# Kernel tuning notes

Measured on AMD Instinct MI355X. Metric: run time of the kernel, lower is better.

## Reference

```python
import jax, jax.numpy as jnp
import numpy as np
import math

N, IN_DIM, OUT_DIM = 4096, 1024, 1024
MASK = True


def setup_inputs() -> dict:
    key = jax.random.key(0)
    ks = jax.random.split(key, 6)
    s = 1.0 / math.sqrt(IN_DIM)
    return {
        "qx": jax.random.normal(ks[0], (N, IN_DIM), jnp.float32),
        "kx": jax.random.normal(ks[1], (N, IN_DIM), jnp.float32),
        "vx": jax.random.normal(ks[2], (N, IN_DIM), jnp.float32),
        # torch nn.Linear weight layout: [out_dim, in_dim], y = x @ W.T
        "Wq": jax.random.normal(ks[3], (OUT_DIM, IN_DIM), jnp.float32) * s,
        "Wk": jax.random.normal(ks[4], (OUT_DIM, IN_DIM), jnp.float32) * s,
        "Wv": jax.random.normal(ks[5], (OUT_DIM, IN_DIM), jnp.float32) * s,
    }


def reference(qx, kx, vx, Wq, Wk, Wv):
    q = qx @ Wq.T  # [n, d]
    k = kx @ Wk.T
    v = vx @ Wv.T
    scores = (q @ k.T) / jnp.float32(math.sqrt(OUT_DIM))  # [n, n]
    if MASK:
        n = qx.shape[0]
        col = jnp.arange(n)[None, :]
        row = jnp.arange(n)[:, None]
        # original: -10000 where j > i (strictly upper triangular)
        scores = scores + jnp.where(col > row, jnp.float32(-10000.0), jnp.float32(0.0))
    attn = jax.nn.softmax(scores, axis=1)
    return attn @ v
```

## Files before the change

### kernel.cpp

```cpp
#include <hip/hip_runtime.h>
#include <hip/hip_bf16.h>
#include <stdint.h>

#define NTOK 4096
#define DIM  1024

typedef unsigned short u16;
typedef __bf16 bf16x8 __attribute__((ext_vector_type(8)));
typedef float f32x4 __attribute__((ext_vector_type(4)));
typedef u16 u16x8 __attribute__((ext_vector_type(8)));

__device__ __forceinline__ u16 f2bf(float f) {
  union { float f; uint32_t u; } c; c.f = f;
  return (u16)((c.u + 0x7fffu + ((c.u >> 16) & 1u)) >> 16);
}
__device__ __forceinline__ float bf2f(u16 b) {
  union { uint32_t u; float f; } c; c.u = (uint32_t)b << 16;
  return c.f;
}

__device__ __forceinline__ float wave_max(float v) {
#pragma unroll
  for (int o = 32; o; o >>= 1) v = fmaxf(v, __shfl_xor(v, o, 64));
  return v;
}
__device__ __forceinline__ float wave_sum(float v) {
#pragma unroll
  for (int o = 32; o; o >>= 1) v += __shfl_xor(v, o, 64);
  return v;
}

__device__ __forceinline__ int xcd_swz(int orig, int nwg) {
  const int q = nwg >> 3, r = nwg & 7;
  const int x = orig & 7, i = orig >> 3;
  return (x < r ? x * (q + 1) : r * (q + 1) + (x - r) * q) + i;
}

__device__ __forceinline__ void gld16(const u16* g, u16* l) {
  __builtin_amdgcn_global_load_lds((const __attribute__((address_space(1))) void*)g,
                                   (__attribute__((address_space(3))) void*)l, 16, 0, 0);
}

template<int N> __device__ __forceinline__ void wait_vmcnt() {
  if constexpr (N == 0) asm volatile("s_waitcnt vmcnt(0)" ::: "memory");
  else if constexpr (N == 6) asm volatile("s_waitcnt vmcnt(6)" ::: "memory");
  else if constexpr (N == 8) asm volatile("s_waitcnt vmcnt(8)" ::: "memory");
}

__global__ __launch_bounds__(256) void cvt6(
    const float* __restrict__ qx, const float* __restrict__ kx, const float* __restrict__ vx,
    const float* __restrict__ Wq, const float* __restrict__ Wk, const float* __restrict__ Wv,
    u16* __restrict__ qxb, u16* __restrict__ kxb, u16* __restrict__ vxb,
    u16* __restrict__ Wqb, u16* __restrict__ Wkb, u16* __restrict__ Wvb)
{
  const int z = blockIdx.z;
  const int nelem = (z < 3) ? NTOK * DIM : DIM * DIM;
  const int i = (blockIdx.x * 256 + threadIdx.x) * 8;
  if (i >= nelem) return;
  const float* in = (z == 0) ? qx : (z == 1) ? kx : (z == 2) ? vx
                  : (z == 3) ? Wq : (z == 4) ? Wk : Wv;
  u16* out = (z == 0) ? qxb : (z == 1) ? kxb : (z == 2) ? vxb
           : (z == 3) ? Wqb : (z == 4) ? Wkb : Wvb;
  float4 a = *reinterpret_cast<const float4*>(in + i);
  float4 b = *reinterpret_cast<const float4*>(in + i + 4);
  u16x8 o;
  o[0] = f2bf(a.x); o[1] = f2bf(a.y); o[2] = f2bf(a.z); o[3] = f2bf(a.w);
  o[4] = f2bf(b.x); o[5] = f2bf(b.y); o[6] = f2bf(b.z); o[7] = f2bf(b.w);
  *reinterpret_cast<u16x8*>(out + i) = o;
}

template<int BM>
__device__ __forceinline__ void mm_core(
    const u16* __restrict__ A, const u16* __restrict__ B,
    int lda, int ldb, int klo, int khi, int row0, int col0,
    u16* sA, u16* sB, f32x4 (&acc)[BM / 32][4])
{
  constexpr int RPWA = BM / 4;
  constexpr int ASZ = BM * 64;
  constexpr int BSZ = 128 * 64;
  constexpr int LPS = BM / 32 + 4;
  const int tid = threadIdx.x;
  const int wave = tid >> 6, lane = tid & 63;
  const int wr = wave >> 1, wc = wave & 1;
  const int l15 = lane & 15, l4 = lane >> 4;
  const int h = l15 & 7;

  const int srow = lane >> 3;
  const int scol = ((lane & 7) ^ (lane >> 3)) << 3;
  const u16* gA = A + (size_t)(row0 + wave * RPWA + srow) * lda + scol;
  const u16* gB = B + (size_t)(col0 + wave * 32 + srow) * ldb + scol;
  const int lbA = wave * RPWA * 64;
  const int lbB = wave * 32 * 64;

  auto stage = [&](int k0, u16* bA, u16* bB) {
#pragma unroll
    for (int i = 0; i < BM / 32; ++i)
      gld16(gA + (size_t)(i * 8) * lda + k0, bA + lbA + i * 512);
#pragma unroll
    for (int i = 0; i < 4; ++i)
      gld16(gB + (size_t)(i * 8) * ldb + k0, bB + lbB + i * 512);
  };

  stage(klo, sA, sB);
  int cur = 0;
  for (int k0 = klo; k0 < khi; k0 += 64) {
    const bool more = (k0 + 64 < khi);
    if (more) {
      stage(k0 + 64, sA + (cur ^ 1) * ASZ, sB + (cur ^ 1) * BSZ);
      wait_vmcnt<LPS>();
    } else {
      wait_vmcnt<0>();
    }
    __builtin_amdgcn_s_barrier();
    __builtin_amdgcn_sched_barrier(0);

    const char* bA = (const char*)(sA + cur * ASZ);
    const char* bB = (const char*)(sB + cur * BSZ);
#pragma unroll
    for (int ks = 0; ks < 2; ++ks) {
      bf16x8 af[BM / 32], bfv[4];
#pragma unroll
      for (int mf = 0; mf < BM / 32; ++mf)
        af[mf] = *reinterpret_cast<const bf16x8*>(
            bA + ((wr * (BM / 2) + mf * 16 + l15) << 7) + ((((ks << 2) + l4) ^ h) << 4));
#pragma unroll
      for (int nf = 0; nf < 4; ++nf)
        bfv[nf] = *reinterpret_cast<const bf16x8*>(
            bB + ((wc * 64 + nf * 16 + l15) << 7) + ((((ks << 2) + l4) ^ h) << 4));
#pragma unroll
      for (int mf = 0; mf < BM / 32; ++mf)
#pragma unroll
        for (int nf = 0; nf < 4; ++nf)
          acc[mf][nf] = __builtin_amdgcn_mfma_f32_16x16x32_bf16(af[mf], bfv[nf], acc[mf][nf], 0, 0, 0);
    }

    __builtin_amdgcn_s_barrier();
    __builtin_amdgcn_sched_barrier(0);
    cur ^= 1;
  }
}

__global__ __launch_bounds__(256) void proj_sw(
    const u16* __restrict__ qxb, const u16* __restrict__ kxb, const u16* __restrict__ vxb,
    const u16* __restrict__ Wqb, const u16* __restrict__ Wkb, const u16* __restrict__ Wvb,
    u16* __restrict__ qb, u16* __restrict__ kb, u16* __restrict__ vT)
{
  __shared__ alignas(16) u16 sA[2 * 128 * 64];
  __shared__ alignas(16) u16 sB[2 * 128 * 64];
  const int w = xcd_swz(blockIdx.x, 768);
  const int z = w >> 8, rem = w & 255;
  const int by = rem >> 3, bx = rem & 7;
  const u16* A = (z == 0) ? qxb : (z == 1) ? kxb : vxb;
  const u16* B = (z == 0) ? Wqb : (z == 1) ? Wkb : Wvb;
  const int row0 = by * 128, col0 = bx * 128;

  f32x4 acc[4][4] = {};
  mm_core<128>(A, B, DIM, DIM, 0, DIM, row0, col0, sA, sB, acc);

  const int lane = threadIdx.x & 63;
  const int wave = threadIdx.x >> 6;
  const int l15 = lane & 15, l4 = lane >> 4;
  const int om = row0 + (wave >> 1) * 64;
  const int on = col0 + (wave & 1) * 64;
  if (z < 2) {
    u16* C = (z == 0) ? qb : kb;
#pragma unroll
    for (int mf = 0; mf < 4; ++mf)
#pragma unroll
      for (int nf = 0; nf < 4; ++nf)
#pragma unroll
        for (int r = 0; r < 4; ++r)
          C[(size_t)(om + mf * 16 + l4 * 4 + r) * DIM + (on + nf * 16 + l15)] = f2bf(acc[mf][nf][r]);
  } else {
#pragma unroll
    for (int mf = 0; mf < 4; ++mf)
#pragma unroll
      for (int nf = 0; nf < 4; ++nf) {
        ushort4 o;
        o.x = f2bf(acc[mf][nf][0]);
        o.y = f2bf(acc[mf][nf][1]);
        o.z = f2bf(acc[mf][nf][2]);
        o.w = f2bf(acc[mf][nf][3]);
        *reinterpret_cast<ushort4*>(&vT[(size_t)(on + nf * 16 + l15) * NTOK + (om + mf * 16 + l4 * 4)]) = o;
      }
  }
}

__global__ __launch_bounds__(256) void gemm_scores(
    const u16* __restrict__ A, const u16* __restrict__ B, u16* __restrict__ C, float scale)
{
  __shared__ alignas(16) u16 sA[2 * 128 * 64];
  __shared__ alignas(16) u16 sB[2 * 128 * 64];
  const int t = xcd_swz(blockIdx.x, 528);
  int by = (int)((sqrtf(8.0f * t + 1.0f) - 1.0f) * 0.5f);
  while ((by + 1) * (by + 2) / 2 <= t) ++by;
  while (by * (by + 1) / 2 > t) --by;
  const int bx = t - by * (by + 1) / 2;
  const int row0 = by * 128, col0 = bx * 128;

  f32x4 acc[4][4] = {};
  mm_core<128>(A, B, DIM, DIM, 0, DIM, row0, col0, sA, sB, acc);

  const int lane = threadIdx.x & 63;
  const int wave = threadIdx.x >> 6;
  const int l15 = lane & 15, l4 = lane >> 4;
  const int om = row0 + (wave >> 1) * 64;
  const int on = col0 + (wave & 1) * 64;
#pragma unroll
  for (int mf = 0; mf < 4; ++mf)
#pragma unroll
    for (int nf = 0; nf < 4; ++nf)
#pragma unroll
      for (int r = 0; r < 4; ++r)
        C[(size_t)(om + mf * 16 + l4 * 4 + r) * NTOK + (on + nf * 16 + l15)] = f2bf(acc[mf][nf][r] * scale);
}

__global__ __launch_bounds__(256) void gemm_pv(
    const u16* __restrict__ P, const u16* __restrict__ vT, float* __restrict__ C)
{
  __shared__ alignas(16) u16 sA[2 * 64 * 64];
  __shared__ alignas(16) u16 sB[2 * 128 * 64];
  const int w = xcd_swz(blockIdx.x, 768);
  const int bx = w & 7;
  const int cid = w >> 3;
  int by, half;
  if (cid < 32) { by = cid; half = -1; }
  else { const int j = cid - 32; by = 32 + (j >> 1); half = j & 1; }
  const int row0 = by * 64, col0 = bx * 128;
  const int Klim = row0 + 64;
  int klo = 0, khi = Klim;
  if (half >= 0) {
    const int h1 = (((Klim >> 6) + 1) >> 1) << 6;
    if (half == 0) khi = h1; else klo = h1;
  }

  f32x4 acc[2][4] = {};
  mm_core<64>(P, vT, NTOK, NTOK, klo, khi, row0, col0, sA, sB, acc);

  const int lane = threadIdx.x & 63;
  const int wave = threadIdx.x >> 6;
  const int l15 = lane & 15, l4 = lane >> 4;
  const int om = row0 + (wave >> 1) * 32;
  const int on = col0 + (wave & 1) * 64;
#pragma unroll
  for (int mf = 0; mf < 2; ++mf)
#pragma unroll
    for (int nf = 0; nf < 4; ++nf)
#pragma unroll
      for (int r = 0; r < 4; ++r) {
        const size_t idx = (size_t)(om + mf * 16 + l4 * 4 + r) * DIM + (on + nf * 16 + l15);
        if (half >= 0) atomicAdd(&C[idx], acc[mf][nf][r]);
        else C[idx] = acc[mf][nf][r];
      }
}

__global__ __launch_bounds__(256) void softmax_causal(const u16* __restrict__ S,
                                                      u16* __restrict__ P) {
  __shared__ float buf[NTOK];
  __shared__ float red[8];
  const int row = blockIdx.x;
  const int tid = threadIdx.x;
  const int limit = row + 1;
  const int limit128 = (row & ~127) + 128;
  const u16* srow = S + (size_t)row * NTOK;

  float lmax = -1e30f;
  for (int j = tid * 8; j < limit128; j += 2048) {
    float v[8];
    if (j + 8 <= limit) {
      u16x8 sv = *reinterpret_cast<const u16x8*>(srow + j);
#pragma unroll
      for (int e = 0; e < 8; ++e) v[e] = bf2f(sv[e]);
    } else {
#pragma unroll
      for (int e = 0; e < 8; ++e) v[e] = (j + e < limit) ? bf2f(srow[j + e]) : -1e30f;
    }
    float4 lo = {v[0], v[1], v[2], v[3]}, hi = {v[4], v[5], v[6], v[7]};
    *reinterpret_cast<float4*>(buf + j) = lo;
    *reinterpret_cast<float4*>(buf + j + 4) = hi;
#pragma unroll
    for (int e = 0; e < 8; ++e) lmax = fmaxf(lmax, v[e]);
  }
  lmax = wave_max(lmax);
  if ((tid & 63) == 0) red[tid >> 6] = lmax;
  __syncthreads();
  const float m = fmaxf(fmaxf(red[0], red[1]), fmaxf(red[2], red[3]));

  float lsum = 0.f;
  for (int j = tid * 8; j < limit128; j += 2048) {
    float4 lo = *reinterpret_cast<float4*>(buf + j);
    float4 hi = *reinterpret_cast<float4*>(buf + j + 4);
    float e0 = __expf(lo.x - m), e1 = __expf(lo.y - m), e2 = __expf(lo.z - m), e3 = __expf(lo.w - m);
    float e4 = __expf(hi.x - m), e5 = __expf(hi.y - m), e6 = __expf(hi.z - m), e7 = __expf(hi.w - m);
    float4 eo = {e0, e1, e2, e3}, eh = {e4, e5, e6, e7};
    *reinterpret_cast<float4*>(buf + j) = eo;
    *reinterpret_cast<float4*>(buf + j + 4) = eh;
    lsum += ((e0 + e1) + (e2 + e3)) + ((e4 + e5) + (e6 + e7));
  }
  lsum = wave_sum(lsum);
  if ((tid & 63) == 0) red[4 + (tid >> 6)] = lsum;
  __syncthreads();
  const float inv = 1.0f / (red[4] + red[5] + red[6] + red[7]);

  u16* prow = P + (size_t)row * NTOK;
  for (int j = tid * 8; j < limit128; j += 2048) {
    float4 lo = *reinterpret_cast<float4*>(buf + j);
    float4 hi = *reinterpret_cast<float4*>(buf + j + 4);
    u16x8 o;
    o[0] = f2bf(lo.x * inv); o[1] = f2bf(lo.y * inv);
    o[2] = f2bf(lo.z * inv); o[3] = f2bf(lo.w * inv);
    o[4] = f2bf(hi.x * inv); o[5] = f2bf(hi.y * inv);
    o[6] = f2bf(hi.z * inv); o[7] = f2bf(hi.w * inv);
    *reinterpret_cast<u16x8*>(prow + j) = o;
  }
}

extern "C" void kernel_launch(void* const* d_in, const int* in_sizes, int n_in,
                              void* d_out, int out_size, void* d_ws, size_t ws_size,
                              hipStream_t stream) {
  const float* qx = (const float*)d_in[0];
  const float* kx = (const float*)d_in[1];
  const float* vx = (const float*)d_in[2];
  const float* Wq = (const float*)d_in[3];
  const float* Wk = (const float*)d_in[4];
  const float* Wv = (const float*)d_in[5];
  float* out = (float*)d_out;
  char* ws = (char*)d_ws;
  const size_t MB = 1024ull * 1024ull;

  if (ws_size < 120 * MB) {
    hipMemsetAsync(d_out, 0xFF, (size_t)out_size * sizeof(float), stream);
    return;
  }

  u16* qxb = (u16*)(ws);
  u16* kxb = (u16*)(ws + 8 * MB);
  u16* vxb = (u16*)(ws + 16 * MB);
  u16* Wqb = (u16*)(ws + 24 * MB);
  u16* Wkb = (u16*)(ws + 26 * MB);
  u16* Wvb = (u16*)(ws + 28 * MB);
  u16* S   = (u16*)(ws);
  u16* qb  = (u16*)(ws + 64 * MB);
  u16* kb  = (u16*)(ws + 72 * MB);
  u16* vT  = (u16*)(ws + 80 * MB);
  u16* P   = (u16*)(ws + 88 * MB);

  hipMemsetAsync((char*)out + (size_t)2048 * DIM * 4, 0, (size_t)2048 * DIM * 4, stream);

  cvt6<<<dim3(NTOK * DIM / (256 * 8), 1, 6), 256, 0, stream>>>(
      qx, kx, vx, Wq, Wk, Wv, qxb, kxb, vxb, Wqb, Wkb, Wvb);

  proj_sw<<<768, 256, 0, stream>>>(qxb, kxb, vxb, Wqb, Wkb, Wvb, qb, kb, vT);

  gemm_scores<<<528, 256, 0, stream>>>(qb, kb, S, 0.03125f);

  softmax_causal<<<NTOK, 256, 0, stream>>>(S, P);

  gemm_pv<<<768, 256, 0, stream>>>(P, vT, out);
}
```

Before: 138.2 us.

## Fuse softmax into score GEMM epilogue and PV GEMM prologue

The score GEMM epilogue now emits per-64-column partial row max and sum-exp statistics. A small combine kernel merges these into a per-row max and inverse sum. The PV GEMM recomputes exp(S - m) on the fly while staging the A tile and scales by the inverse sum in the epilogue. This removes the standalone softmax pass and the P buffer round trip. In exchange the PV loop loses its double-buffered async A staging, using synchronous loads plus exp work with two barriers per K step, which may expose latency.

After: 181.7 us. 31.4% more time.

```diff
diff --git a/kernel.cpp b/kernel.cpp
--- a/kernel.cpp
+++ b/kernel.cpp
@@ -17,17 +17,6 @@
 __device__ __forceinline__ float bf2f(u16 b) {
   union { uint32_t u; float f; } c; c.u = (uint32_t)b << 16;
   return c.f;
-}
-
-__device__ __forceinline__ float wave_max(float v) {
-#pragma unroll
-  for (int o = 32; o; o >>= 1) v = fmaxf(v, __shfl_xor(v, o, 64));
-  return v;
-}
-__device__ __forceinline__ float wave_sum(float v) {
-#pragma unroll
-  for (int o = 32; o; o >>= 1) v += __shfl_xor(v, o, 64);
-  return v;
 }
 
 __device__ __forceinline__ int xcd_swz(int orig, int nwg) {
@@ -69,16 +58,12 @@
   *reinterpret_cast<u16x8*>(out + i) = o;
 }
 
-template<int BM>
-__device__ __forceinline__ void mm_core(
+__device__ __forceinline__ void mm128(
     const u16* __restrict__ A, const u16* __restrict__ B,
     int lda, int ldb, int klo, int khi, int row0, int col0,
-    u16* sA, u16* sB, f32x4 (&acc)[BM / 32][4])
-{
-  constexpr int RPWA = BM / 4;
-  constexpr int ASZ = BM * 64;
-  constexpr int BSZ = 128 * 64;
-  constexpr int LPS = BM / 32 + 4;
+    u16* sA, u16* sB, f32x4 (&acc)[4][4])
+{
+  constexpr int ASZ = 128 * 64, BSZ = 128 * 64;
   const int tid = threadIdx.x;
   const int wave = tid >> 6, lane = tid & 63;
   const int wr = wave >> 1, wc = wave & 1;
@@ -87,14 +72,14 @@
 
   const int srow = lane >> 3;
   const int scol = ((lane & 7) ^ (lane >> 3)) << 3;
-  const u16* gA = A + (size_t)(row0 + wave * RPWA + srow) * lda + scol;
+  const u16* gA = A + (size_t)(row0 + wave * 32 + srow) * lda + scol;
   const u16* gB = B + (size_t)(col0 + wave * 32 + srow) * ldb + scol;
-  const int lbA = wave * RPWA * 64;
+  const int lbA = wave * 32 * 64;
   const int lbB = wave * 32 * 64;
 
   auto stage = [&](int k0, u16* bA, u16* bB) {
 #pragma unroll
-    for (int i = 0; i < BM / 32; ++i)
+    for (int i = 0; i < 4; ++i)
       gld16(gA + (size_t)(i * 8) * lda + k0, bA + lbA + i * 512);
 #pragma unroll
     for (int i = 0; i < 4; ++i)
@@ -107,7 +92,7 @@
     const bool more = (k0 + 64 < khi);
     if (more) {
       stage(k0 + 64, sA + (cur ^ 1) * ASZ, sB + (cur ^ 1) * BSZ);
-      wait_vmcnt<LPS>();
+      wait_vmcnt<8>();
     } else {
       wait_vmcnt<0>();
     }
@@ -118,17 +103,17 @@
     const char* bB = (const char*)(sB + cur * BSZ);
 #pragma unroll
     for (int ks = 0; ks < 2; ++ks) {
-      bf16x8 af[BM / 32], bfv[4];
-#pragma unroll
-      for (int mf = 0; mf < BM / 32; ++mf)
+      bf16x8 af[4], bfv[4];
+#pragma unroll
+      for (int mf = 0; mf < 4; ++mf)
         af[mf] = *reinterpret_cast<const bf16x8*>(
-            bA + ((wr * (BM / 2) + mf * 16 + l15) << 7) + ((((ks << 2) + l4) ^ h) << 4));
+            bA + ((wr * 64 + mf * 16 + l15) << 7) + ((((ks << 2) + l4) ^ h) << 4));
 #pragma unroll
       for (int nf = 0; nf < 4; ++nf)
         bfv[nf] = *reinterpret_cast<const bf16x8*>(
             bB + ((wc * 64 + nf * 16 + l15) << 7) + ((((ks << 2) + l4) ^ h) << 4));
 #pragma unroll
-      for (int mf = 0; mf < BM / 32; ++mf)
+      for (int mf = 0; mf < 4; ++mf)
 #pragma unroll
         for (int nf = 0; nf < 4; ++nf)
           acc[mf][nf] = __builtin_amdgcn_mfma_f32_16x16x32_bf16(af[mf], bfv[nf], acc[mf][nf], 0, 0, 0);
@@ -155,7 +140,7 @@
   const int row0 = by * 128, col0 = bx * 128;
 
   f32x4 acc[4][4] = {};
-  mm_core<128>(A, B, DIM, DIM, 0, DIM, row0, col0, sA, sB, acc);
+  mm128(A, B, DIM, DIM, 0, DIM, row0, col0, sA, sB, acc);
 
   const int lane = threadIdx.x & 63;
   const int wave = threadIdx.x >> 6;
@@ -187,7 +172,8 @@
 }
 
 __global__ __launch_bounds__(256) void gemm_scores(
-    const u16* __restrict__ A, const u16* __restrict__ B, u16* __restrict__ C, float scale)
+    const u16* __restrict__ A, const u16* __restrict__ B, u16* __restrict__ C,
+    float* __restrict__ Mp, float* __restrict__ Lp, float scale)
 {
   __shared__ alignas(16) u16 sA[2 * 128 * 64];
   __shared__ alignas(16) u16 sB[2 * 128 * 64];
@@ -199,27 +185,69 @@
   const int row0 = by * 128, col0 = bx * 128;
 
   f32x4 acc[4][4] = {};
-  mm_core<128>(A, B, DIM, DIM, 0, DIM, row0, col0, sA, sB, acc);
+  mm128(A, B, DIM, DIM, 0, DIM, row0, col0, sA, sB, acc);
 
   const int lane = threadIdx.x & 63;
   const int wave = threadIdx.x >> 6;
   const int l15 = lane & 15, l4 = lane >> 4;
   const int om = row0 + (wave >> 1) * 64;
   const int on = col0 + (wave & 1) * 64;
+  const int g = on >> 6;
+
 #pragma unroll
   for (int mf = 0; mf < 4; ++mf)
 #pragma unroll
-    for (int nf = 0; nf < 4; ++nf)
-#pragma unroll
-      for (int r = 0; r < 4; ++r)
-        C[(size_t)(om + mf * 16 + l4 * 4 + r) * NTOK + (on + nf * 16 + l15)] = f2bf(acc[mf][nf][r] * scale);
+    for (int r = 0; r < 4; ++r) {
+      const int row = om + mf * 16 + l4 * 4 + r;
+      float s[4];
+      bool valid[4];
+#pragma unroll
+      for (int nf = 0; nf < 4; ++nf) {
+        const int col = on + nf * 16 + l15;
+        s[nf] = acc[mf][nf][r] * scale;
+        valid[nf] = (col <= row);
+        C[(size_t)row * NTOK + col] = f2bf(s[nf]);
+      }
+      float mx = -1e30f;
+#pragma unroll
+      for (int nf = 0; nf < 4; ++nf) mx = valid[nf] ? fmaxf(mx, s[nf]) : mx;
+#pragma unroll
+      for (int o = 1; o < 16; o <<= 1) mx = fmaxf(mx, __shfl_xor(mx, o, 64));
+      float es = 0.f;
+#pragma unroll
+      for (int nf = 0; nf < 4; ++nf) es += valid[nf] ? __expf(s[nf] - mx) : 0.f;
+#pragma unroll
+      for (int o = 1; o < 16; o <<= 1) es += __shfl_xor(es, o, 64);
+      if (l15 == 0) {
+        Mp[(size_t)row * 64 + g] = mx;
+        Lp[(size_t)row * 64 + g] = es;
+      }
+    }
+}
+
+__global__ __launch_bounds__(256) void combine_stats(
+    const float* __restrict__ Mp, const float* __restrict__ Lp,
+    float* __restrict__ M, float* __restrict__ Linv)
+{
+  const int row = blockIdx.x * 256 + threadIdx.x;
+  const int nt = (row >> 6) + 1;
+  const float* mp = Mp + (size_t)row * 64;
+  const float* lp = Lp + (size_t)row * 64;
+  float m = -1e30f;
+  for (int t = 0; t < nt; ++t) m = fmaxf(m, mp[t]);
+  float l = 0.f;
+  for (int t = 0; t < nt; ++t) l += lp[t] * __expf(mp[t] - m);
+  M[row] = m;
+  Linv[row] = 1.0f / l;
 }
 
 __global__ __launch_bounds__(256) void gemm_pv(
-    const u16* __restrict__ P, const u16* __restrict__ vT, float* __restrict__ C)
-{
-  __shared__ alignas(16) u16 sA[2 * 64 * 64];
-  __shared__ alignas(16) u16 sB[2 * 128 * 64];
+    const u16* __restrict__ S, const u16* __restrict__ vT,
+    const float* __restrict__ M, const float* __restrict__ Linv,
+    float* __restrict__ C)
+{
+  __shared__ alignas(16) u16 sA[64 * 64];
+  __shared__ alignas(16) u16 sB[128 * 64];
   const int w = xcd_swz(blockIdx.x, 768);
   const int bx = w & 7;
   const int cid = w >> 3;
@@ -234,85 +262,81 @@
     if (half == 0) khi = h1; else klo = h1;
   }
 
+  const int tid = threadIdx.x;
+  const int wave = tid >> 6, lane = tid & 63;
+  const int wr = wave >> 1, wc = wave & 1;
+  const int l15 = lane & 15, l4 = lane >> 4;
+  const int h = l15 & 7;
+
+  const int srow = lane >> 3;
+  const int scol = ((lane & 7) ^ (lane >> 3)) << 3;
+  const int ar0 = row0 + wave * 16 + srow;
+  const int ar1 = ar0 + 8;
+  const u16* gA = S + (size_t)ar0 * NTOK + scol;
+  const u16* gB = vT + (size_t)(col0 + wave * 32 + srow) * NTOK + scol;
+  const int lbA = wave * 16 * 64;
+  const int lbB = wave * 32 * 64;
+  const float m0 = M[ar0], m1 = M[ar1];
+
   f32x4 acc[2][4] = {};
-  mm_core<64>(P, vT, NTOK, NTOK, klo, khi, row0, col0, sA, sB, acc);
-
-  const int lane = threadIdx.x & 63;
-  const int wave = threadIdx.x >> 6;
-  const int l15 = lane & 15, l4 = lane >> 4;
-  const int om = row0 + (wave >> 1) * 32;
-  const int on = col0 + (wave & 1) * 64;
+
+  for (int k0 = klo; k0 < khi; k0 += 64) {
+    __syncthreads();
+#pragma unroll
+    for (int i = 0; i < 4; ++i)
+      gld16(gB + (size_t)(i * 8) * NTOK + k0, &sB[lbB + i * 8 * 64]);
+    u16x8 s0 = *reinterpret_cast<const u16x8*>(gA + k0);
+    u16x8 s1 = *reinterpret_cast<const u16x8*>(gA + (size_t)8 * NTOK + k0);
+    u16x8 p0, p1;
+#pragma unroll
+    for (int e = 0; e < 8; ++e) {
+      const int col = k0 + scol + e;
+      const float pa = __expf(bf2f(s0[e]) - m0);
+      const float pb = __expf(bf2f(s1[e]) - m1);
+      p0[e] = (col <= ar0) ? f2bf(pa) : (u16)0;
+      p1[e] = (col <= ar1) ? f2bf(pb) : (u16)0;
+    }
+    *reinterpret_cast<u16x8*>(&sA[lbA + lane * 8]) = p0;
+    *reinterpret_cast<u16x8*>(&sA[lbA + 512 + lane * 8]) = p1;
+    __syncthreads();
+#pragma unroll
+    for (int ks = 0; ks < 2; ++ks) {
+      bf16x8 af[2], bfv[4];
+#pragma unroll
+      for (int mf = 0; mf < 2; ++mf)
+        af[mf] = *reinterpret_cast<const bf16x8*>(
+            (const char*)sA + ((wr * 32 + mf * 16 + l15) << 7) + ((((ks << 2) + l4) ^ h) << 4));
+#pragma unroll
+      for (int nf = 0; nf < 4; ++nf)
+        bfv[nf] = *reinterpret_cast<const bf16x8*>(
+            (const char*)sB + ((wc * 64 + nf * 16 + l15) << 7) + ((((ks << 2) + l4) ^ h) << 4));
+#pragma unroll
+      for (int mf = 0; mf < 2; ++mf)
+#pragma unroll
+        for (int nf = 0; nf < 4; ++nf)
+          acc[mf][nf] = __builtin_amdgcn_mfma_f32_16x16x32_bf16(af[mf], bfv[nf], acc[mf][nf], 0, 0, 0);
+    }
+  }
+
+  const int om = row0 + wr * 32;
+  const int on = col0 + wc * 64;
+  float linv[2][4];
 #pragma unroll
   for (int mf = 0; mf < 2; ++mf)
 #pragma unroll
+    for (int r = 0; r < 4; ++r)
+      linv[mf][r] = Linv[om + mf * 16 + l4 * 4 + r];
+#pragma unroll
+  for (int mf = 0; mf < 2; ++mf)
+#pragma unroll
     for (int nf = 0; nf < 4; ++nf)
 #pragma unroll
       for (int r = 0; r < 4; ++r) {
+        const float v = acc[mf][nf][r] * linv[mf][r];
         const size_t idx = (size_t)(om + mf * 16 + l4 * 4 + r) * DIM + (on + nf * 16 + l15);
-        if (half >= 0) atomicAdd(&C[idx], acc[mf][nf][r]);
-        else C[idx] = acc[mf][nf][r];
+        if (half >= 0) atomicAdd(&C[idx], v);
+        else C[idx] = v;
       }
-}
-
-__global__ __launch_bounds__(256) void softmax_causal(const u16* __restrict__ S,
-                                                      u16* __restrict__ P) {
-  __shared__ float buf[NTOK];
-  __shared__ float red[8];
-  const int row = blockIdx.x;
-  const int tid = threadIdx.x;
-  const int limit = row + 1;
-  const int limit128 = (row & ~127) + 128;
-  const u16* srow = S + (size_t)row * NTOK;
-
-  float lmax = -1e30f;
-  for (int j = tid * 8; j < limit128; j += 2048) {
-    float v[8];
-    if (j + 8 <= limit) {
-      u16x8 sv = *reinterpret_cast<const u16x8*>(srow + j);
-#pragma unroll
-      for (int e = 0; e < 8; ++e) v[e] = bf2f(sv[e]);
-    } else {
-#pragma unroll
-      for (int e = 0; e < 8; ++e) v[e] = (j + e < limit) ? bf2f(srow[j + e]) : -1e30f;
-    }
-    float4 lo = {v[0], v[1], v[2], v[3]}, hi = {v[4], v[5], v[6], v[7]};
-    *reinterpret_cast<float4*>(buf + j) = lo;
-    *reinterpret_cast<float4*>(buf + j + 4) = hi;
-#pragma unroll
-    for (int e = 0; e < 8; ++e) lmax = fmaxf(lmax, v[e]);
-  }
-  lmax = wave_max(lmax);
-  if ((tid & 63) == 0) red[tid >> 6] = lmax;
-  __syncthreads();
-  const float m = fmaxf(fmaxf(red[0], red[1]), fmaxf(red[2], red[3]));
-
-  float lsum = 0.f;
-  for (int j = tid * 8; j < limit128; j += 2048) {
-    float4 lo = *reinterpret_cast<float4*>(buf + j);
-    float4 hi = *reinterpret_cast<float4*>(buf + j + 4);
-    float e0 = __expf(lo.x - m), e1 = __expf(lo.y - m), e2 = __expf(lo.z - m), e3 = __expf(lo.w - m);
-    float e4 = __expf(hi.x - m), e5 = __expf(hi.y - m), e6 = __expf(hi.z - m), e7 = __expf(hi.w - m);
-    float4 eo = {e0, e1, e2, e3}, eh = {e4, e5, e6, e7};
-    *reinterpret_cast<float4*>(buf + j) = eo;
-    *reinterpret_cast<float4*>(buf + j + 4) = eh;
-    lsum += ((e0 + e1) + (e2 + e3)) + ((e4 + e5) + (e6 + e7));
-  }
-  lsum = wave_sum(lsum);
-  if ((tid & 63) == 0) red[4 + (tid >> 6)] = lsum;
-  __syncthreads();
-  const float inv = 1.0f / (red[4] + red[5] + red[6] + red[7]);
-
-  u16* prow = P + (size_t)row * NTOK;
-  for (int j = tid * 8; j < limit128; j += 2048) {
-    float4 lo = *reinterpret_cast<float4*>(buf + j);
-    float4 hi = *reinterpret_cast<float4*>(buf + j + 4);
-    u16x8 o;
-    o[0] = f2bf(lo.x * inv); o[1] = f2bf(lo.y * inv);
-    o[2] = f2bf(lo.z * inv); o[3] = f2bf(lo.w * inv);
-    o[4] = f2bf(hi.x * inv); o[5] = f2bf(hi.y * inv);
-    o[6] = f2bf(hi.z * inv); o[7] = f2bf(hi.w * inv);
-    *reinterpret_cast<u16x8*>(prow + j) = o;
-  }
 }
 
 extern "C" void kernel_launch(void* const* d_in, const int* in_sizes, int n_in,
@@ -340,10 +364,13 @@
   u16* Wkb = (u16*)(ws + 26 * MB);
   u16* Wvb = (u16*)(ws + 28 * MB);
   u16* S   = (u16*)(ws);
+  float* Mp   = (float*)(ws + 32 * MB);
+  float* Lp   = (float*)(ws + 33 * MB);
+  float* M    = (float*)(ws + 34 * MB);
+  float* Linv = (float*)(ws + 35 * MB);
   u16* qb  = (u16*)(ws + 64 * MB);
   u16* kb  = (u16*)(ws + 72 * MB);
   u16* vT  = (u16*)(ws + 80 * MB);
-  u16* P   = (u16*)(ws + 88 * MB);
 
   hipMemsetAsync((char*)out + (size_t)2048 * DIM * 4, 0, (size_t)2048 * DIM * 4, stream);
 
@@ -352,9 +379,9 @@
 
   proj_sw<<<768, 256, 0, stream>>>(qxb, kxb, vxb, Wqb, Wkb, Wvb, qb, kb, vT);
 
-  gemm_scores<<<528, 256, 0, stream>>>(qb, kb, S, 0.03125f);
-
-  softmax_causal<<<NTOK, 256, 0, stream>>>(S, P);
-
-  gemm_pv<<<768, 256, 0, stream>>>(P, vT, out);
-}
+  gemm_scores<<<528, 256, 0, stream>>>(qb, kb, S, Mp, Lp, 0.03125f);
+
+  combine_stats<<<NTOK / 256, 256, 0, stream>>>(Mp, Lp, M, Linv);
+
+  gemm_pv<<<768, 256, 0, stream>>>(S, vT, M, Linv, out);
+}
```

## Use 256x256 tiles with 8-wave pipelined GEMM for projection and scores

Applied to the files above, without the earlier changes.

Replaces the 128x128 tile, 4-wave GEMM core for the QKV projection and causal score kernels with a 256x256 tile, 8-wave core. The new core splits each K-step into four quadrant MFMA phases that interleave LDS reads with async global-to-LDS prefetch of later tiles, and raises MFMA issue priority during compute. The aim is more data reuse per loaded byte and better overlap of memory with matrix math. In exchange it launches far fewer blocks (192 and 136 on 256 CUs), which risks idle compute units and load imbalance on the triangular score grid.

New measurement: 131.6 us. -4.8%, faster.

```diff
diff --git a/kernel.cpp b/kernel.cpp
--- a/kernel.cpp
+++ b/kernel.cpp
@@ -46,6 +46,12 @@
   else if constexpr (N == 6) asm volatile("s_waitcnt vmcnt(6)" ::: "memory");
   else if constexpr (N == 8) asm volatile("s_waitcnt vmcnt(8)" ::: "memory");
 }
+
+#define SFENCE() __builtin_amdgcn_sched_barrier(0)
+#define BARF()   do { SFENCE(); __builtin_amdgcn_s_barrier(); SFENCE(); } while (0)
+#define LGKM0F() do { SFENCE(); asm volatile("s_waitcnt lgkmcnt(0)" ::: "memory"); SFENCE(); } while (0)
+#define VMC6F()  do { SFENCE(); asm volatile("s_waitcnt vmcnt(6)" ::: "memory"); SFENCE(); } while (0)
+#define VMC0F()  do { SFENCE(); asm volatile("s_waitcnt vmcnt(0)" ::: "memory"); SFENCE(); } while (0)
 
 __global__ __launch_bounds__(256) void cvt6(
     const float* __restrict__ qx, const float* __restrict__ kx, const float* __restrict__ vx,
@@ -69,16 +75,199 @@
   *reinterpret_cast<u16x8*>(out + i) = o;
 }
 
-template<int BM>
-__device__ __forceinline__ void mm_core(
+__device__ __forceinline__ void mm256(
+    const u16* __restrict__ A, const u16* __restrict__ B,
+    int lda, int ldb, int row0, int col0, int nt,
+    u16* lds, f32x4 (&acc)[8][4])
+{
+  const int tid = threadIdx.x;
+  const int wv = tid >> 6, lane = tid & 63;
+  const int wm = wv >> 2, wn = wv & 3;
+  const int l15 = lane & 15, l4 = lane >> 4;
+  const int r8 = lane >> 3;
+  const int gch = ((lane & 7) ^ r8) << 3;
+
+  const int aStrip = wv >> 2;
+  const int aSub   = (wv & 3) * 16;
+  const int bStrip = wv >> 1;
+  const int bSub   = (wv & 1) * 16;
+
+  auto stageA = [&](int parity, int mh, int kt) {
+    const int kofs = kt << 6;
+#pragma unroll
+    for (int jj = 0; jj < 2; ++jj) {
+      const int rr = aSub + jj * 8;
+      const int grow = row0 + aStrip * 128 + mh * 64 + rr + r8;
+      u16* d = lds + parity * 32768 + mh * 8192 + aStrip * 4096 + rr * 64;
+      gld16(A + (size_t)grow * lda + gch + kofs, d);
+    }
+  };
+  auto stageB = [&](int parity, int nh, int kt) {
+    const int kofs = kt << 6;
+#pragma unroll
+    for (int jj = 0; jj < 2; ++jj) {
+      const int rr = bSub + jj * 8;
+      const int grow = col0 + bStrip * 64 + nh * 32 + rr + r8;
+      u16* d = lds + parity * 32768 + 16384 + nh * 8192 + bStrip * 2048 + rr * 64;
+      gld16(B + (size_t)grow * ldb + gch + kofs, d);
+    }
+  };
+
+  bf16x8 af[4][2];
+  bf16x8 bfr[2][2][2];
+
+  auto read_af = [&](int parity, int mh) {
+#pragma unroll
+    for (int mf = 0; mf < 4; ++mf)
+#pragma unroll
+      for (int ks = 0; ks < 2; ++ks) {
+        const int rr = mf * 16 + l15;
+        af[mf][ks] = *reinterpret_cast<const bf16x8*>(
+            lds + parity * 32768 + mh * 8192 + wm * 4096 + rr * 64 +
+            ((((ks << 2) + l4) ^ (rr & 7)) << 3));
+      }
+  };
+  auto read_bf = [&](int parity, int nh) {
+#pragma unroll
+    for (int nf = 0; nf < 2; ++nf)
+#pragma unroll
+      for (int ks = 0; ks < 2; ++ks) {
+        const int rr = nf * 16 + l15;
+        bfr[nh][nf][ks] = *reinterpret_cast<const bf16x8*>(
+            lds + parity * 32768 + 16384 + nh * 8192 + wn * 2048 + rr * 64 +
+            ((((ks << 2) + l4) ^ (rr & 7)) << 3));
+      }
+  };
+  auto quad = [&](int mh, int nh) {
+    __builtin_amdgcn_s_setprio(1);
+#pragma unroll
+    for (int mf = 0; mf < 4; ++mf)
+#pragma unroll
+      for (int nf = 0; nf < 2; ++nf)
+#pragma unroll
+        for (int ks = 0; ks < 2; ++ks)
+          acc[mh * 4 + mf][nh * 2 + nf] = __builtin_amdgcn_mfma_f32_16x16x32_bf16(
+              af[mf][ks], bfr[nh][nf][ks], acc[mh * 4 + mf][nh * 2 + nf], 0, 0, 0);
+    __builtin_amdgcn_s_setprio(0);
+  };
+
+  stageA(0, 0, 0); SFENCE();
+  stageA(0, 1, 0); SFENCE();
+  stageB(0, 0, 0); SFENCE();
+  stageB(0, 1, 0); SFENCE();
+  const int t1 = (nt > 1) ? 1 : 0;
+  stageA(1, 0, t1); SFENCE();
+  stageB(1, 0, t1); SFENCE();
+  stageB(1, 1, t1); SFENCE();
+  VMC0F();
+  BARF();
+
+  for (int t = 0; t < nt; ++t) {
+    const int par = t & 1, nxt = par ^ 1;
+    const int tp1 = (t + 1 < nt) ? t + 1 : nt - 1;
+    const int tp2 = (t + 2 < nt) ? t + 2 : nt - 1;
+    read_af(par, 0); read_bf(par, 0);
+    stageA(nxt, 1, tp1);
+    BARF(); LGKM0F();
+    quad(0, 0);
+    BARF();
+    read_bf(par, 1);
+    stageA(par, 0, tp2);
+    BARF(); LGKM0F();
+    quad(0, 1);
+    BARF();
+    read_af(par, 1);
+    stageB(par, 0, tp2);
+    BARF(); LGKM0F();
+    quad(1, 0);
+    BARF();
+    stageB(par, 1, tp2);
+    VMC6F();
+    BARF();
+    quad(1, 1);
+    BARF();
+  }
+
+  VMC0F();
+}
+
+__global__ __launch_bounds__(512, 2) void proj256(
+    const u16* __restrict__ qxb, const u16* __restrict__ kxb, const u16* __restrict__ vxb,
+    const u16* __restrict__ Wqb, const u16* __restrict__ Wkb, const u16* __restrict__ Wvb,
+    u16* __restrict__ qb, u16* __restrict__ kb, u16* __restrict__ vT)
+{
+  __shared__ alignas(16) u16 lds[65536];
+  const int w = xcd_swz(blockIdx.x, 192);
+  const int z = w >> 6, rem = w & 63;
+  const int by = rem >> 2, bx = rem & 3;
+  const u16* A = (z == 0) ? qxb : (z == 1) ? kxb : vxb;
+  const u16* B = (z == 0) ? Wqb : (z == 1) ? Wkb : Wvb;
+  const int row0 = by * 256, col0 = bx * 256;
+
+  f32x4 acc[8][4] = {};
+  mm256(A, B, DIM, DIM, row0, col0, DIM / 64, lds, acc);
+
+  const int wv = threadIdx.x >> 6, lane = threadIdx.x & 63;
+  const int wm = wv >> 2, wn = wv & 3;
+  const int l15 = lane & 15, l4 = lane >> 4;
+  const int om = row0 + wm * 128;
+  const int on = col0 + wn * 64;
+  if (z < 2) {
+    u16* C = (z == 0) ? qb : kb;
+#pragma unroll
+    for (int m = 0; m < 8; ++m)
+#pragma unroll
+      for (int n = 0; n < 4; ++n)
+#pragma unroll
+        for (int r = 0; r < 4; ++r)
+          C[(size_t)(om + m * 16 + l4 * 4 + r) * DIM + (on + n * 16 + l15)] = f2bf(acc[m][n][r]);
+  } else {
+#pragma unroll
+    for (int m = 0; m < 8; ++m)
+#pragma unroll
+      for (int n = 0; n < 4; ++n) {
+        ushort4 o;
+        o.x = f2bf(acc[m][n][0]); o.y = f2bf(acc[m][n][1]);
+        o.z = f2bf(acc[m][n][2]); o.w = f2bf(acc[m][n][3]);
+        *reinterpret_cast<ushort4*>(&vT[(size_t)(on + n * 16 + l15) * NTOK + (om + m * 16 + l4 * 4)]) = o;
+      }
+  }
+}
+
+__global__ __launch_bounds__(512, 2) void scores256(
+    const u16* __restrict__ A, const u16* __restrict__ B, u16* __restrict__ C, float scale)
+{
+  __shared__ alignas(16) u16 lds[65536];
+  const int t = xcd_swz(blockIdx.x, 136);
+  int by = (int)((sqrtf(8.0f * t + 1.0f) - 1.0f) * 0.5f);
+  while ((by + 1) * (by + 2) / 2 <= t) ++by;
+  while (by * (by + 1) / 2 > t) --by;
+  const int bx = t - by * (by + 1) / 2;
+  const int row0 = by * 256, col0 = bx * 256;
+
+  f32x4 acc[8][4] = {};
+  mm256(A, B, DIM, DIM, row0, col0, DIM / 64, lds, acc);
+
+  const int wv = threadIdx.x >> 6, lane = threadIdx.x & 63;
+  const int wm = wv >> 2, wn = wv & 3;
+  const int l15 = lane & 15, l4 = lane >> 4;
+  const int om = row0 + wm * 128;
+  const int on = col0 + wn * 64;
+#pragma unroll
+  for (int m = 0; m < 8; ++m)
+#pragma unroll
+    for (int n = 0; n < 4; ++n)
+#pragma unroll
+      for (int r = 0; r < 4; ++r)
+        C[(size_t)(om + m * 16 + l4 * 4 + r) * NTOK + (on + n * 16 + l15)] = f2bf(acc[m][n][r] * scale);
+}
+
+__device__ __forceinline__ void mm64(
     const u16* __restrict__ A, const u16* __restrict__ B,
     int lda, int ldb, int klo, int khi, int row0, int col0,
-    u16* sA, u16* sB, f32x4 (&acc)[BM / 32][4])
-{
-  constexpr int RPWA = BM / 4;
-  constexpr int ASZ = BM * 64;
-  constexpr int BSZ = 128 * 64;
-  constexpr int LPS = BM / 32 + 4;
+    u16* sA, u16* sB, f32x4 (&acc)[2][4])
+{
+  constexpr int ASZ = 64 * 64, BSZ = 128 * 64;
   const int tid = threadIdx.x;
   const int wave = tid >> 6, lane = tid & 63;
   const int wr = wave >> 1, wc = wave & 1;
@@ -87,14 +276,14 @@
 
   const int srow = lane >> 3;
   const int scol = ((lane & 7) ^ (lane >> 3)) << 3;
-  const u16* gA = A + (size_t)(row0 + wave * RPWA + srow) * lda + scol;
+  const u16* gA = A + (size_t)(row0 + wave * 16 + srow) * lda + scol;
   const u16* gB = B + (size_t)(col0 + wave * 32 + srow) * ldb + scol;
-  const int lbA = wave * RPWA * 64;
+  const int lbA = wave * 16 * 64;
   const int lbB = wave * 32 * 64;
 
   auto stage = [&](int k0, u16* bA, u16* bB) {
 #pragma unroll
-    for (int i = 0; i < BM / 32; ++i)
+    for (int i = 0; i < 2; ++i)
       gld16(gA + (size_t)(i * 8) * lda + k0, bA + lbA + i * 512);
 #pragma unroll
     for (int i = 0; i < 4; ++i)
@@ -107,112 +296,38 @@
     const bool more = (k0 + 64 < khi);
     if (more) {
       stage(k0 + 64, sA + (cur ^ 1) * ASZ, sB + (cur ^ 1) * BSZ);
-      wait_vmcnt<LPS>();
+      SFENCE(); wait_vmcnt<6>(); SFENCE();
     } else {
-      wait_vmcnt<0>();
+      SFENCE(); wait_vmcnt<0>(); SFENCE();
     }
     __builtin_amdgcn_s_barrier();
-    __builtin_amdgcn_sched_barrier(0);
+    SFENCE();
 
     const char* bA = (const char*)(sA + cur * ASZ);
     const char* bB = (const char*)(sB + cur * BSZ);
 #pragma unroll
     for (int ks = 0; ks < 2; ++ks) {
-      bf16x8 af[BM / 32], bfv[4];
-#pragma unroll
-      for (int mf = 0; mf < BM / 32; ++mf)
+      bf16x8 af[2], bfv[4];
+#pragma unroll
+      for (int mf = 0; mf < 2; ++mf)
         af[mf] = *reinterpret_cast<const bf16x8*>(
-            bA + ((wr * (BM / 2) + mf * 16 + l15) << 7) + ((((ks << 2) + l4) ^ h) << 4));
+            bA + ((wr * 32 + mf * 16 + l15) << 7) + ((((ks << 2) + l4) ^ h) << 4));
 #pragma unroll
       for (int nf = 0; nf < 4; ++nf)
         bfv[nf] = *reinterpret_cast<const bf16x8*>(
             bB + ((wc * 64 + nf * 16 + l15) << 7) + ((((ks << 2) + l4) ^ h) << 4));
 #pragma unroll
-      for (int mf = 0; mf < BM / 32; ++mf)
+      for (int mf = 0; mf < 2; ++mf)
 #pragma unroll
         for (int nf = 0; nf < 4; ++nf)
           acc[mf][nf] = __builtin_amdgcn_mfma_f32_16x16x32_bf16(af[mf], bfv[nf], acc[mf][nf], 0, 0, 0);
     }
 
+    SFENCE();
     __builtin_amdgcn_s_barrier();
-    __builtin_amdgcn_sched_barrier(0);
+    SFENCE();
     cur ^= 1;
   }
-}
-
-__global__ __launch_bounds__(256) void proj_sw(
-    const u16* __restrict__ qxb, const u16* __restrict__ kxb, const u16* __restrict__ vxb,
-    const u16* __restrict__ Wqb, const u16* __restrict__ Wkb, const u16* __restrict__ Wvb,
-    u16* __restrict__ qb, u16* __restrict__ kb, u16* __restrict__ vT)
-{
-  __shared__ alignas(16) u16 sA[2 * 128 * 64];
-  __shared__ alignas(16) u16 sB[2 * 128 * 64];
-  const int w = xcd_swz(blockIdx.x, 768);
-  const int z = w >> 8, rem = w & 255;
-  const int by = rem >> 3, bx = rem & 7;
-  const u16* A = (z == 0) ? qxb : (z == 1) ? kxb : vxb;
-  const u16* B = (z == 0) ? Wqb : (z == 1) ? Wkb : Wvb;
-  const int row0 = by * 128, col0 = bx * 128;
-
-  f32x4 acc[4][4] = {};
-  mm_core<128>(A, B, DIM, DIM, 0, DIM, row0, col0, sA, sB, acc);
-
-  const int lane = threadIdx.x & 63;
-  const int wave = threadIdx.x >> 6;
-  const int l15 = lane & 15, l4 = lane >> 4;
-  const int om = row0 + (wave >> 1) * 64;
-  const int on = col0 + (wave & 1) * 64;
-  if (z < 2) {
-    u16* C = (z == 0) ? qb : kb;
-#pragma unroll
-    for (int mf = 0; mf < 4; ++mf)
-#pragma unroll
-      for (int nf = 0; nf < 4; ++nf)
-#pragma unroll
-        for (int r = 0; r < 4; ++r)
-          C[(size_t)(om + mf * 16 + l4 * 4 + r) * DIM + (on + nf * 16 + l15)] = f2bf(acc[mf][nf][r]);
-  } else {
-#pragma unroll
-    for (int mf = 0; mf < 4; ++mf)
-#pragma unroll
-      for (int nf = 0; nf < 4; ++nf) {
-        ushort4 o;
-        o.x = f2bf(acc[mf][nf][0]);
-        o.y = f2bf(acc[mf][nf][1]);
-        o.z = f2bf(acc[mf][nf][2]);
-        o.w = f2bf(acc[mf][nf][3]);
-        *reinterpret_cast<ushort4*>(&vT[(size_t)(on + nf * 16 + l15) * NTOK + (om + mf * 16 + l4 * 4)]) = o;
-      }
-  }
-}
-
-__global__ __launch_bounds__(256) void gemm_scores(
-    const u16* __restrict__ A, const u16* __restrict__ B, u16* __restrict__ C, float scale)
-{
-  __shared__ alignas(16) u16 sA[2 * 128 * 64];
-  __shared__ alignas(16) u16 sB[2 * 128 * 64];
-  const int t = xcd_swz(blockIdx.x, 528);
-  int by = (int)((sqrtf(8.0f * t + 1.0f) - 1.0f) * 0.5f);
-  while ((by + 1) * (by + 2) / 2 <= t) ++by;
-  while (by * (by + 1) / 2 > t) --by;
-  const int bx = t - by * (by + 1) / 2;
-  const int row0 = by * 128, col0 = bx * 128;
-
-  f32x4 acc[4][4] = {};
-  mm_core<128>(A, B, DIM, DIM, 0, DIM, row0, col0, sA, sB, acc);
-
-  const int lane = threadIdx.x & 63;
-  const int wave = threadIdx.x >> 6;
-  const int l15 = lane & 15, l4 = lane >> 4;
-  const int om = row0 + (wave >> 1) * 64;
-  const int on = col0 + (wave & 1) * 64;
-#pragma unroll
-  for (int mf = 0; mf < 4; ++mf)
-#pragma unroll
-    for (int nf = 0; nf < 4; ++nf)
-#pragma unroll
-      for (int r = 0; r < 4; ++r)
-        C[(size_t)(om + mf * 16 + l4 * 4 + r) * NTOK + (on + nf * 16 + l15)] = f2bf(acc[mf][nf][r] * scale);
 }
 
 __global__ __launch_bounds__(256) void gemm_pv(
@@ -235,7 +350,7 @@
   }
 
   f32x4 acc[2][4] = {};
-  mm_core<64>(P, vT, NTOK, NTOK, klo, khi, row0, col0, sA, sB, acc);
+  mm64(P, vT, NTOK, NTOK, klo, khi, row0, col0, sA, sB, acc);
 
   const int lane = threadIdx.x & 63;
   const int wave = threadIdx.x >> 6;
@@ -350,9 +465,9 @@
   cvt6<<<dim3(NTOK * DIM / (256 * 8), 1, 6), 256, 0, stream>>>(
       qx, kx, vx, Wq, Wk, Wv, qxb, kxb, vxb, Wqb, Wkb, Wvb);
 
-  proj_sw<<<768, 256, 0, stream>>>(qxb, kxb, vxb, Wqb, Wkb, Wvb, qb, kb, vT);
-
-  gemm_scores<<<528, 256, 0, stream>>>(qb, kb, S, 0.03125f);
+  proj256<<<192, 512, 0, stream>>>(qxb, kxb, vxb, Wqb, Wkb, Wvb, qb, kb, vT);
+
+  scores256<<<136, 512, 0, stream>>>(qb, kb, S, 0.03125f);
 
   softmax_causal<<<NTOK, 256, 0, stream>>>(S, P);
 
```
